# Kernel tuning notes

Hardware: AMD Instinct MI355X
Metric: run time of the kernel (lower is better)

Reference implementation:

```python
import jax, jax.numpy as jnp
import numpy as np

NUM_HEADS = 12


def setup_inputs() -> dict:
    key = jax.random.key(0)
    ks = jax.random.split(key, 6)
    B, F, P, C = 2, 8, 196, 768
    N = 1 + F * P
    s = 0.02
    return {
        "x": jax.random.normal(ks[0], (B, N, C), jnp.float32),
        "Wqkv": jax.random.normal(ks[1], (C, 3 * C), jnp.float32) * s,
        "Wq": jax.random.normal(ks[2], (C, C), jnp.float32) * s,
        "Wkv": jax.random.normal(ks[3], (C, 2 * C), jnp.float32) * s,
        "Wproj": jax.random.normal(ks[4], (C, C), jnp.float32) * s,
        "bproj": jnp.zeros((C,), jnp.float32),
        "seq_len": 196,
        "num_frames": 8,
    }


def reference(x, Wqkv, Wq, Wkv, Wproj, bproj, seq_len, num_frames):
    B, N, C = x.shape
    H = NUM_HEADS
    d = C // H
    scale = d ** -0.5
    F, P = num_frames, seq_len
    S = F * P  # N == 1 + S

    qkv = x @ Wqkv                                # [B, N, 3C]
    q, k, v = jnp.split(qkv, 3, axis=-1)
    def to_heads(t):  # [B, N, C] -> [B*H, N, d]
        return t.reshape(B, N, H, d).transpose(0, 2, 1, 3).reshape(B * H, N, d)
    q, k, v = to_heads(q), to_heads(k), to_heads(v)

    # --- cls token attends over everything ---
    cls_q = q[:, :1] * scale                      # [BH, 1, d]
    cls_attn = jax.nn.softmax(jnp.einsum('bid,bjd->bij', cls_q, k), axis=-1)
    cls_out = jnp.einsum('bij,bjd->bid', cls_attn, v)  # [BH, 1, d]
    cls_out = cls_out.reshape(B, H, d).reshape(B, 1, C)

    # --- per-frame spatial softmax ---
    q_, k_, v_ = q[:, 1:], k[:, 1:], v[:, 1:]     # [BH, S, d]
    qk = jnp.einsum('bqd,bkd->bqk', q_, k_).reshape(B * H, S, F, P)
    sp_attn = jax.nn.softmax(scale * qk, axis=-1)  # softmax over patches within frame
    v_f = v_.reshape(B * H, F, P, d)
    xt = jnp.einsum('bqfn,bfnd->bqfd', sp_attn, v_f)  # [BH, S, F, d]

    x4 = xt.reshape(B, H, S, F, d).transpose(0, 2, 3, 1, 4).reshape(B, S, F, C)

    # --- diagonal extraction: query frame g == key frame f ---
    x5 = x4.reshape(B, F, P, F, C)
    xd = jnp.diagonal(x5, axis1=1, axis2=3)       # [B, P, C, F]
    xd = xd.transpose(0, 3, 1, 2).reshape(B, S, C)

    # --- temporal trajectory attention ---
    q2 = (xd @ Wq).reshape(B, S, H, d).transpose(0, 2, 1, 3) * scale  # [B,H,S,d]
    kv2 = x4 @ Wkv                                # [B, S, F, 2C]
    k2 = kv2[..., :C].reshape(B, S, F, H, d).transpose(0, 3, 1, 2, 4)  # [B,H,S,F,d]
    attn2 = jax.nn.softmax(jnp.einsum('bhsd,bhsfd->bhsf', q2, k2), axis=-1)
    # use_original_code=True: aggregate the trajectory tensor x4 itself
    xr = x4.reshape(B, S, F, H, d).transpose(0, 3, 1, 2, 4)            # [B,H,S,F,d]
    out = jnp.einsum('bhsf,bhsfd->bhsd', attn2, xr)
    out = out.transpose(0, 2, 1, 3).reshape(B, S, C)

    out = jnp.concatenate([cls_out, out], axis=1) @ Wproj + bproj      # [B, N, C]
    return out, attn2
```

## Files before the change

### kernel.cpp

```cpp
#include <hip/hip_runtime.h>

namespace {
constexpr int kB = 2;
constexpr int kH = 12;
constexpr int kD = 64;
constexpr int kC = 768;
constexpr int kF = 8;
constexpr int kP = 196;
constexpr int kS = kF * kP;
constexpr int kN = 1 + kS;
constexpr int k3C = 3 * kC;
constexpr float kScale = 0.125f;
constexpr int kBH = kB * kH;
constexpr int kPpad = 224;
constexpr int kLpad = 1600;
constexpr int kBS = kB * kS;
}

typedef __attribute__((ext_vector_type(8))) short bf16x8;
typedef __attribute__((ext_vector_type(8))) unsigned short u16x8;
typedef __attribute__((ext_vector_type(4))) float f32x4;
typedef __attribute__((ext_vector_type(4))) unsigned int u32x4;

__device__ inline ushort f2bf(float x) {
  union { float f; unsigned u; } v{x};
  unsigned r = v.u + 0x7fff + ((v.u >> 16) & 1);
  return (ushort)(r >> 16);
}
__device__ inline float bf2f(ushort u) {
  union { unsigned u; float f; } v{(unsigned)u << 16};
  return v.f;
}

__device__ __forceinline__ void gload_lds16(const void* g, void* l) {
  __builtin_amdgcn_global_load_lds(
      (const __attribute__((address_space(1))) unsigned int*)g,
      (__attribute__((address_space(3))) unsigned int*)l, 16, 0, 0);
}

__device__ inline void storeC(float v, float* p) { *p = v; }
__device__ inline void storeC(float v, ushort* p) { *p = f2bf(v); }

template <typename OutT>
__global__ __launch_bounds__(256) void gemm_bf16(
    const ushort* __restrict__ A, const ushort* __restrict__ Bt,
    const float* __restrict__ bias, OutT* __restrict__ C,
    int M, int N, int K, int nbx) {
  const int nwg = gridDim.x;
  const int q = nwg >> 3, rr = nwg & 7;
  const int xcd = blockIdx.x & 7, loc = blockIdx.x >> 3;
  const int vid = ((xcd < rr) ? xcd * (q + 1) : rr * (q + 1) + (xcd - rr) * q) + loc;
  const int m0 = (vid / nbx) * 128, n0 = (vid % nbx) * 128;

  __shared__ __align__(16) ushort As[128 * 32];
  __shared__ __align__(16) ushort Bs[128 * 32];
  const int tid = threadIdx.x;
  const int r0 = tid >> 2, c0 = tid & 3;
  const int r1 = r0 + 64;
  const int sc0 = (c0 ^ ((r0 >> 1) & 3)) * 8;
  const int sc1 = (c0 ^ ((r1 >> 1) & 3)) * 8;
  const int ar0 = min(m0 + r0, M - 1), ar1 = min(m0 + r1, M - 1);
  const ushort* ga0 = A + (size_t)ar0 * K + sc0;
  const ushort* ga1 = A + (size_t)ar1 * K + sc1;
  const ushort* gb0 = Bt + (size_t)(n0 + r0) * K + sc0;
  const ushort* gb1 = Bt + (size_t)(n0 + r1) * K + sc1;
  const int w = tid >> 6;
  char* lA0 = (char*)As + w * 1024;
  char* lA1 = (char*)As + 4096 + w * 1024;
  char* lB0 = (char*)Bs + w * 1024;
  char* lB1 = (char*)Bs + 4096 + w * 1024;
  const int lane = tid & 63;
  const int lr = lane & 15, lg = lane >> 4;
  const int wr = w >> 1, wc = w & 1;
  f32x4 acc[4][4] = {};
  for (int kt = 0; kt < K; kt += 32) {
    gload_lds16(ga0 + kt, lA0);
    gload_lds16(ga1 + kt, lA1);
    gload_lds16(gb0 + kt, lB0);
    gload_lds16(gb1 + kt, lB1);
    __syncthreads();
    bf16x8 af[4], bfr[4];
#pragma unroll
    for (int m = 0; m < 4; ++m) {
      int row = wr * 64 + m * 16 + lr;
      int ch = lg ^ ((row >> 1) & 3);
      af[m] = *(const bf16x8*)(As + row * 32 + ch * 8);
    }
#pragma unroll
    for (int n = 0; n < 4; ++n) {
      int row = wc * 64 + n * 16 + lr;
      int ch = lg ^ ((row >> 1) & 3);
      bfr[n] = *(const bf16x8*)(Bs + row * 32 + ch * 8);
    }
#pragma unroll
    for (int m = 0; m < 4; ++m)
#pragma unroll
      for (int n = 0; n < 4; ++n)
        acc[m][n] =
            __builtin_amdgcn_mfma_f32_16x16x32_bf16(af[m], bfr[n], acc[m][n], 0, 0, 0);
    __syncthreads();
  }
#pragma unroll
  for (int m = 0; m < 4; ++m) {
#pragma unroll
    for (int r = 0; r < 4; ++r) {
      const int mg = m0 + wr * 64 + m * 16 + lg * 4 + r;
      if (mg < M) {
        OutT* crow = C + (size_t)mg * N + n0 + wc * 64 + lr;
#pragma unroll
        for (int n = 0; n < 4; ++n) {
          float v = acc[m][n][r];
          if (bias) v += bias[n0 + wc * 64 + n * 16 + lr];
          storeC(v, crow + n * 16);
        }
      }
    }
  }
}

__global__ __launch_bounds__(256) void w2_gemm(
    const ushort* __restrict__ q2b, const ushort* __restrict__ Wkvb,
    ushort* __restrict__ w2b) {
  const int nwg = gridDim.x;
  const int q = nwg >> 3, rr = nwg & 7;
  const int xcd = blockIdx.x & 7, loc = blockIdx.x >> 3;
  const int vid = ((xcd < rr) ? xcd * (q + 1) : rr * (q + 1) + (xcd - rr) * q) + loc;
  const int h = vid / 150;
  const int rem = vid - h * 150;
  const int m0 = (rem / 6) * 128, n0 = (rem % 6) * 128;

  __shared__ __align__(16) ushort As[128 * 32];
  __shared__ __align__(16) ushort Bs[128 * 32];
  const int tid = threadIdx.x;
  const int r0 = tid >> 2, c0 = tid & 3;
  const int r1 = r0 + 64;
  const int sc0 = (c0 ^ ((r0 >> 1) & 3)) * 8;
  const int sc1 = (c0 ^ ((r1 >> 1) & 3)) * 8;
  const int ar0 = min(m0 + r0, kBS - 1), ar1 = min(m0 + r1, kBS - 1);
  const ushort* ga0 = q2b + (size_t)ar0 * kC + h * 64 + sc0;
  const ushort* ga1 = q2b + (size_t)ar1 * kC + h * 64 + sc1;
  const ushort* gb0 = Wkvb + (size_t)(n0 + r0) * kC + h * 64 + sc0;
  const ushort* gb1 = Wkvb + (size_t)(n0 + r1) * kC + h * 64 + sc1;
  const int w = tid >> 6;
  char* lA0 = (char*)As + w * 1024;
  char* lA1 = (char*)As + 4096 + w * 1024;
  char* lB0 = (char*)Bs + w * 1024;
  char* lB1 = (char*)Bs + 4096 + w * 1024;
  const int lane = tid & 63;
  const int lr = lane & 15, lg = lane >> 4;
  const int wr = w >> 1, wc = w & 1;
  f32x4 acc[4][4] = {};
#pragma unroll
  for (int kt = 0; kt < 64; kt += 32) {
    gload_lds16(ga0 + kt, lA0);
    gload_lds16(ga1 + kt, lA1);
    gload_lds16(gb0 + kt, lB0);
    gload_lds16(gb1 + kt, lB1);
    __syncthreads();
    bf16x8 af[4], bfr[4];
#pragma unroll
    for (int m = 0; m < 4; ++m) {
      int row = wr * 64 + m * 16 + lr;
      int ch = lg ^ ((row >> 1) & 3);
      af[m] = *(const bf16x8*)(As + row * 32 + ch * 8);
    }
#pragma unroll
    for (int n = 0; n < 4; ++n) {
      int row = wc * 64 + n * 16 + lr;
      int ch = lg ^ ((row >> 1) & 3);
      bfr[n] = *(const bf16x8*)(Bs + row * 32 + ch * 8);
    }
#pragma unroll
    for (int m = 0; m < 4; ++m)
#pragma unroll
      for (int n = 0; n < 4; ++n)
        acc[m][n] =
            __builtin_amdgcn_mfma_f32_16x16x32_bf16(af[m], bfr[n], acc[m][n], 0, 0, 0);
    __syncthreads();
  }
#pragma unroll
  for (int m = 0; m < 4; ++m) {
#pragma unroll
    for (int r = 0; r < 4; ++r) {
      const int mg = m0 + wr * 64 + m * 16 + lg * 4 + r;
      if (mg < kBS) {
        ushort* crow = w2b + (size_t)mg * (kH * kC) + h * kC + n0 + wc * 64 + lr;
#pragma unroll
        for (int n = 0; n < 4; ++n) crow[n * 16] = f2bf(acc[m][n][r]);
      }
    }
  }
}

__global__ void pack_x_k(const float* __restrict__ X, ushort* __restrict__ Xb,
                         int n4) {
  const int i = blockIdx.x * 256 + threadIdx.x;
  if (i >= n4) return;
  float4 v = ((const float4*)X)[i];
  ushort4 o = {f2bf(v.x), f2bf(v.y), f2bf(v.z), f2bf(v.w)};
  ((ushort4*)Xb)[i] = o;
}

__global__ __launch_bounds__(256) void pack_wt_k(const float* __restrict__ W,
                                                 ushort* __restrict__ Wt,
                                                 int ldw, float scale) {
  __shared__ float t[32][33];
  const int nb = blockIdx.x * 32;
  const int kb = blockIdx.y * 32;
  const int tx = threadIdx.x & 31, ty = threadIdx.x >> 5;
#pragma unroll
  for (int i = 0; i < 32; i += 8)
    t[ty + i][tx] = W[(size_t)(kb + ty + i) * ldw + nb + tx];
  __syncthreads();
#pragma unroll
  for (int i = 0; i < 32; i += 8)
    Wt[(size_t)(nb + ty + i) * 768 + kb + tx] = f2bf(t[tx][ty + i] * scale);
}

__global__ void pack_wkv_k(const float* __restrict__ Wkv,
                           ushort* __restrict__ Wkvb) {
  const int i = blockIdx.x * 256 + threadIdx.x;
  if (i >= 768 * 192) return;
  const int c = i / 192, j4 = i - c * 192;
  float4 v = *(const float4*)(Wkv + (size_t)c * 1536 + j4 * 4);
  ushort4 o = {f2bf(v.x), f2bf(v.y), f2bf(v.z), f2bf(v.w)};
  *(ushort4*)(Wkvb + (size_t)c * 768 + j4 * 4) = o;
}

__global__ void pack_qk_k(const ushort* __restrict__ qkvb,
                          ushort* __restrict__ Qb, ushort* __restrict__ Kb) {
  const int idx = blockIdx.x * 256 + threadIdx.x;
  if (idx >= kBH * kS * 8) return;
  const int j8 = idx & 7;
  const int s = (idx >> 3) % kS;
  const int bh = idx / (kS * 8);
  const int b = bh / kH, h = bh % kH;
  const size_t src = (size_t)(b * kN + 1 + s) * k3C + h * kD + j8 * 8;
  u16x8 qv = *(const u16x8*)(qkvb + src);
  u16x8 qo;
#pragma unroll
  for (int j = 0; j < 8; ++j) qo[j] = f2bf(bf2f(qv[j]) * kScale);
  const size_t dst = ((size_t)bh * kS + s) * kD + j8 * 8;
  *(u16x8*)(Qb + dst) = qo;
  *(u16x8*)(Kb + dst) = *(const u16x8*)(qkvb + src + kC);
}

__global__ void pack_vt_k(const ushort* __restrict__ qkvb,
                          ushort* __restrict__ Vt) {
  const int idx = blockIdx.x * 256 + threadIdx.x;
  if (idx >= kBH * kF * kD * kPpad) return;
  const int n = idx % kPpad;
  const int j = (idx / kPpad) & 63;
  const int f = (idx / (kPpad * kD)) & 7;
  const int bh = idx / (kPpad * kD * kF);
  const int b = bh / kH, h = bh % kH;
  ushort v = 0;
  if (n < kP)
    v = qkvb[(size_t)(b * kN + 1 + f * kP + n) * k3C + 2 * kC + h * kD + j];
  Vt[idx] = v;
}

__global__ __launch_bounds__(256) void sp_attn_mfma(
    const ushort* __restrict__ Qb, const ushort* __restrict__ Kb,
    const ushort* __restrict__ Vt, ushort* __restrict__ x4b) {
  const int w = threadIdx.x >> 6;
  const int lane = threadIdx.x & 63;
  const int fbh = blockIdx.x;
  const int f = fbh / 24, bh = fbh % 24;
  const int tile = blockIdx.y * 4 + w;
  if (tile >= 49) return;
  const int q0 = tile * 32;
  const int lr = lane & 15;
  const int lg = lane >> 4;

  const ushort* qrow = Qb + ((size_t)bh * kS + q0 + lr) * kD + lg * 8;
  const bf16x8 a00 = *(const bf16x8*)qrow;
  const bf16x8 a01 = *(const bf16x8*)(qrow + 32);
  const bf16x8 a10 = *(const bf16x8*)(qrow + 16 * kD);
  const bf16x8 a11 = *(const bf16x8*)(qrow + 16 * kD + 32);

  f32x4 s0[13], s1[13];
  const ushort* kbase = Kb + ((size_t)bh * kS + f * kP + lr) * kD + lg * 8;
#pragma unroll
  for (int nt = 0; nt < 13; ++nt) {
    const ushort* kr = kbase + (size_t)nt * 16 * kD;
    bf16x8 b0 = *(const bf16x8*)kr;
    bf16x8 b1 = *(const bf16x8*)(kr + 32);
    f32x4 acc0 = {0.f, 0.f, 0.f, 0.f}, acc1 = {0.f, 0.f, 0.f, 0.f};
    acc0 = __builtin_amdgcn_mfma_f32_16x16x32_bf16(b0, a00, acc0, 0, 0, 0);
    acc0 = __builtin_amdgcn_mfma_f32_16x16x32_bf16(b1, a01, acc0, 0, 0, 0);
    acc1 = __builtin_amdgcn_mfma_f32_16x16x32_bf16(b0, a10, acc1, 0, 0, 0);
    acc1 = __builtin_amdgcn_mfma_f32_16x16x32_bf16(b1, a11, acc1, 0, 0, 0);
    s0[nt] = acc0;
    s1[nt] = acc1;
  }
  if (lg >= 1) {
#pragma unroll
    for (int r = 0; r < 4; ++r) { s0[12][r] = -1e30f; s1[12][r] = -1e30f; }
  }

  float m0 = -1e30f, m1 = -1e30f;
#pragma unroll
  for (int nt = 0; nt < 13; ++nt)
#pragma unroll
    for (int r = 0; r < 4; ++r) {
      m0 = fmaxf(m0, s0[nt][r]);
      m1 = fmaxf(m1, s1[nt][r]);
    }
  m0 = fmaxf(m0, __shfl_xor(m0, 16));
  m0 = fmaxf(m0, __shfl_xor(m0, 32));
  m1 = fmaxf(m1, __shfl_xor(m1, 16));
  m1 = fmaxf(m1, __shfl_xor(m1, 32));

  float sum0 = 0.f, sum1 = 0.f;
  u32x4 breg0[7], breg1[7];
#pragma unroll
  for (int blk = 0; blk < 7; ++blk) {
    unsigned pk0[2][2], pk1[2][2];
#pragma unroll
    for (int t = 0; t < 2; ++t) {
      const int nt = blk * 2 + t;
      if (nt < 13) {
        float e0 = __expf(s0[nt][0] - m0), e1 = __expf(s0[nt][1] - m0);
        float e2 = __expf(s0[nt][2] - m0), e3 = __expf(s0[nt][3] - m0);
        sum0 += (e0 + e1) + (e2 + e3);
        pk0[t][0] = ((unsigned)f2bf(e1) << 16) | f2bf(e0);
        pk0[t][1] = ((unsigned)f2bf(e3) << 16) | f2bf(e2);
        float g0 = __expf(s1[nt][0] - m1), g1 = __expf(s1[nt][1] - m1);
        float g2 = __expf(s1[nt][2] - m1), g3 = __expf(s1[nt][3] - m1);
        sum1 += (g0 + g1) + (g2 + g3);
        pk1[t][0] = ((unsigned)f2bf(g1) << 16) | f2bf(g0);
        pk1[t][1] = ((unsigned)f2bf(g3) << 16) | f2bf(g2);
      } else {
        pk0[t][0] = 0; pk0[t][1] = 0;
        pk1[t][0] = 0; pk1[t][1] = 0;
      }
    }
#pragma unroll
    for (int j2 = 0; j2 < 4; ++j2) {
      const int srcLane = ((lg & 1) * 2 + (j2 >> 1)) * 16 + lr;
      unsigned t0 = (unsigned)__shfl((int)pk0[0][j2 & 1], srcLane);
      unsigned t1 = (unsigned)__shfl((int)pk0[1][j2 & 1], srcLane);
      breg0[blk][j2] = (lg < 2) ? t0 : t1;
      unsigned u0 = (unsigned)__shfl((int)pk1[0][j2 & 1], srcLane);
      unsigned u1 = (unsigned)__shfl((int)pk1[1][j2 & 1], srcLane);
      breg1[blk][j2] = (lg < 2) ? u0 : u1;
    }
  }
  sum0 += __shfl_xor(sum0, 16);
  sum0 += __shfl_xor(sum0, 32);
  sum1 += __shfl_xor(sum1, 16);
  sum1 += __shfl_xor(sum1, 32);
  const float inv0 = 1.f / sum0, inv1 = 1.f / sum1;

  const ushort* vbase = Vt + ((size_t)(bh * kF + f) * kD + lr) * kPpad + lg * 8;
  f32x4 o0[4] = {}, o1[4] = {};
#pragma unroll
  for (int nt2 = 0; nt2 < 4; ++nt2) {
    const ushort* vb = vbase + (size_t)nt2 * 16 * kPpad;
#pragma unroll
    for (int blk = 0; blk < 7; ++blk) {
      bf16x8 av = *(const bf16x8*)(vb + blk * 32);
      bf16x8 pb0 = __builtin_bit_cast(bf16x8, breg0[blk]);
      bf16x8 pb1 = __builtin_bit_cast(bf16x8, breg1[blk]);
      o0[nt2] = __builtin_amdgcn_mfma_f32_16x16x32_bf16(av, pb0, o0[nt2], 0, 0, 0);
      o1[nt2] = __builtin_amdgcn_mfma_f32_16x16x32_bf16(av, pb1, o1[nt2], 0, 0, 0);
    }
  }

  const int b = bh / kH, h = bh % kH;
  const size_t base0 =
      ((size_t)(b * kS + q0 + lr) * kF + f) * kC + h * kD + lg * 4;
#pragma unroll
  for (int nt2 = 0; nt2 < 4; ++nt2) {
    ushort4 v0, v1;
    v0.x = f2bf(o0[nt2][0] * inv0);
    v0.y = f2bf(o0[nt2][1] * inv0);
    v0.z = f2bf(o0[nt2][2] * inv0);
    v0.w = f2bf(o0[nt2][3] * inv0);
    *(ushort4*)(x4b + base0 + nt2 * 16) = v0;
    v1.x = f2bf(o1[nt2][0] * inv1);
    v1.y = f2bf(o1[nt2][1] * inv1);
    v1.z = f2bf(o1[nt2][2] * inv1);
    v1.w = f2bf(o1[nt2][3] * inv1);
    *(ushort4*)(x4b + base0 + (size_t)16 * kF * kC + nt2 * 16) = v1;
  }
}

__global__ __launch_bounds__(256) void cls_logits_k(const ushort* __restrict__ qkvb,
                                                    float* __restrict__ logits) {
  const int chunk = blockIdx.x, bh = blockIdx.y;
  const int b = bh / kH, h = bh % kH;
  const int g = threadIdx.x & 15, row = threadIdx.x >> 4;
  const size_t base = (size_t)b * kN * k3C;
  const ushort* qp = qkvb + base + h * kD + g * 4;
  const float q0 = bf2f(qp[0]) * kScale, q1 = bf2f(qp[1]) * kScale;
  const float q2 = bf2f(qp[2]) * kScale, q3 = bf2f(qp[3]) * kScale;
#pragma unroll
  for (int i = 0; i < 16; ++i) {
    const int n = chunk * 256 + i * 16 + row;
    if (n < kN) {
      ushort4 kv =
          *(const ushort4*)(qkvb + base + (size_t)n * k3C + kC + h * kD + g * 4);
      float p = q0 * bf2f(kv.x) + q1 * bf2f(kv.y) + q2 * bf2f(kv.z) +
                q3 * bf2f(kv.w);
#pragma unroll
      for (int o = 8; o; o >>= 1) p += __shfl_xor(p, o, 16);
      if (g == 0) logits[bh * kLpad + n] = p;
    }
  }
}

__global__ __launch_bounds__(256) void cls_softmax_k(const float* __restrict__ logits,
                                                     float* __restrict__ pbuf) {
  __shared__ float red[8];
  const int bh = blockIdx.x, tid = threadIdx.x;
  float m = -1e30f;
  for (int n = tid; n < kN; n += 256) m = fmaxf(m, logits[bh * kLpad + n]);
#pragma unroll
  for (int o = 32; o; o >>= 1) m = fmaxf(m, __shfl_xor(m, o));
  if ((tid & 63) == 0) red[tid >> 6] = m;
  __syncthreads();
  m = fmaxf(fmaxf(red[0], red[1]), fmaxf(red[2], red[3]));
  float sum = 0.f;
  for (int n = tid; n < kN; n += 256) sum += __expf(logits[bh * kLpad + n] - m);
#pragma unroll
  for (int o = 32; o; o >>= 1) sum += __shfl_xor(sum, o);
  if ((tid & 63) == 0) red[4 + (tid >> 6)] = sum;
  __syncthreads();
  const float inv = 1.f / (red[4] + red[5] + red[6] + red[7]);
  for (int n = tid; n < kN; n += 256)
    pbuf[bh * kLpad + n] = __expf(logits[bh * kLpad + n] - m) * inv;
}

__global__ __launch_bounds__(256) void cls_pv_k(const ushort* __restrict__ qkvb,
                                                const float* __restrict__ pbuf,
                                                float* __restrict__ partial) {
  __shared__ float pb[256];
  const int chunk = blockIdx.x, bh = blockIdx.y;
  const int b = bh / kH, h = bh % kH;
  const int j = threadIdx.x & 63, part = threadIdx.x >> 6;
  const size_t base = (size_t)b * kN * k3C + 2 * kC + h * kD + j;
  float acc = 0.f;
#pragma unroll 4
  for (int i = 0; i < 64; ++i) {
    const int n = chunk * 256 + i * 4 + part;
    if (n < kN)
      acc = fmaf(pbuf[bh * kLpad + n], bf2f(qkvb[base + (size_t)n * k3C]), acc);
  }
  pb[threadIdx.x] = acc;
  __syncthreads();
  if (part == 0)
    partial[((size_t)bh * 7 + chunk) * kD + j] =
        pb[j] + pb[64 + j] + pb[128 + j] + pb[192 + j];
}

__global__ void cls_red_k(const float* __restrict__ partial,
                          ushort* __restrict__ xin_b) {
  const int bh = blockIdx.x, j = threadIdx.x;
  const int b = bh / kH, h = bh % kH;
  float s = 0.f;
#pragma unroll
  for (int c = 0; c < 7; ++c) s += partial[((size_t)bh * 7 + c) * kD + j];
  xin_b[(size_t)(b * kN) * kC + h * kD + j] = f2bf(s);
}

__global__ void xd_gather_k(const ushort* __restrict__ x4b,
                            ushort* __restrict__ xd_b) {
  const int idx = blockIdx.x * 256 + threadIdx.x;
  const int total = kB * kS * (kC / 8);
  if (idx >= total) return;
  const int row = idx / (kC / 8);
  const int cg = idx - row * (kC / 8);
  const int b = row / kS, s = row - b * kS;
  const int fq = s / kP;
  ((ulonglong2*)xd_b)[(size_t)row * (kC / 8) + cg] =
      ((const ulonglong2*)x4b)[((size_t)(b * kS + s) * kF + fq) * (kC / 8) + cg];
}

__global__ __launch_bounds__(256) void attn2_fused(
    const ushort* __restrict__ x4b, const ushort* __restrict__ w2b,
    ushort* __restrict__ xin_b, float* __restrict__ attn2out) {
  __shared__ __align__(16) ushort x4s[kF * kC];
  __shared__ __align__(16) ushort w2s[kH * kC];
  const int bs = blockIdx.x;
  const int b = bs / kS, s = bs - b * kS;
  const int tid = threadIdx.x;
  {
    const ulonglong2* src = (const ulonglong2*)(x4b + (size_t)bs * kF * kC);
    ulonglong2* dst = (ulonglong2*)x4s;
    for (int i = tid; i < kF * kC / 8; i += 256) dst[i] = src[i];
    const ulonglong2* srcw = (const ulonglong2*)(w2b + (size_t)bs * kH * kC);
    ulonglong2* dstw = (ulonglong2*)w2s;
    for (int i = tid; i < kH * kC / 8; i += 256) dstw[i] = srcw[i];
  }
  __syncthreads();
  const int w = tid >> 6, lane = tid & 63;
#pragma unroll
  for (int hh = 0; hh < 3; ++hh) {
    const int h = w * 3 + hh;
    float part[kF] = {};
#pragma unroll
    for (int i = 0; i < 3; ++i) {
      const int c = lane * 4 + i * 256;
      ushort4 wv = *(const ushort4*)&w2s[h * kC + c];
      const float w0 = bf2f(wv.x), w1 = bf2f(wv.y);
      const float w2v = bf2f(wv.z), w3 = bf2f(wv.w);
#pragma unroll
      for (int f = 0; f < kF; ++f) {
        ushort4 xv = *(const ushort4*)&x4s[f * kC + c];
        part[f] += bf2f(xv.x) * w0 + bf2f(xv.y) * w1 + bf2f(xv.z) * w2v +
                   bf2f(xv.w) * w3;
      }
    }
    float l[kF];
#pragma unroll
    for (int f = 0; f < kF; ++f) {
      float p = part[f];
#pragma unroll
      for (int o = 32; o; o >>= 1) p += __shfl_xor(p, o);
      l[f] = p;
    }
    float m = l[0];
#pragma unroll
    for (int f = 1; f < kF; ++f) m = fmaxf(m, l[f]);
    float sum = 0.f;
#pragma unroll
    for (int f = 0; f < kF; ++f) {
      l[f] = __expf(l[f] - m);
      sum += l[f];
    }
    const float inv = 1.f / sum;
    float pv = 0.f;
#pragma unroll
    for (int f = 0; f < kF; ++f) pv = (lane == f) ? l[f] : pv;
    if (lane < kF)
      attn2out[((size_t)(b * kH + h) * kS + s) * kF + lane] = pv * inv;
    float o = 0.f;
#pragma unroll
    for (int f = 0; f < kF; ++f)
      o = fmaf(l[f] * inv, bf2f(x4s[f * kC + h * kD + lane]), o);
    xin_b[(size_t)(b * kN + 1 + s) * kC + h * kD + lane] = f2bf(o);
  }
}

extern "C" void kernel_launch(void* const* d_in, const int* in_sizes, int n_in,
                              void* d_out, int out_size, void* d_ws,
                              size_t ws_size, hipStream_t stream) {
  const float* x = (const float*)d_in[0];
  const float* Wqkv = (const float*)d_in[1];
  const float* Wq = (const float*)d_in[2];
  const float* Wkv = (const float*)d_in[3];
  const float* Wproj = (const float*)d_in[4];
  const float* bproj = (const float*)d_in[5];

  char* p = (char*)d_ws;
  ushort* qkvb = (ushort*)p;         p += (size_t)3138 * 2304 * 2;
  ushort* w2b = (ushort*)p;          p += (size_t)kBS * kH * kC * 2;
  ushort* q2b = (ushort*)p;          p += (size_t)kBS * kC * 2;
  ushort* x4b = (ushort*)p;          p += (size_t)25088 * 768 * 2;
  ushort* xin_b = (ushort*)p;        p += (size_t)3138 * 768 * 2;
  ushort* xd_b = (ushort*)p;         p += (size_t)kBS * 768 * 2;
  ushort* xb = (ushort*)p;           p += (size_t)3138 * 768 * 2;
  ushort* Wqkv_t = (ushort*)p;       p += (size_t)2304 * 768 * 2;
  ushort* Wq_t = (ushort*)p;         p += (size_t)768 * 768 * 2;
  ushort* Wkvb = (ushort*)p;         p += (size_t)768 * 768 * 2;
  ushort* Wproj_t = (ushort*)p;      p += (size_t)768 * 768 * 2;
  ushort* Qb = (ushort*)p;           p += (size_t)kBH * kS * kD * 2;
  ushort* Kb = (ushort*)p;           p += ((size_t)kBH * kS + 16) * kD * 2;
  ushort* Vt = (ushort*)p;           p += (size_t)kBH * kF * kD * kPpad * 2;
  float* clsL = (float*)p;           p += (size_t)kBH * kLpad * 4;
  float* clsP = (float*)p;           p += (size_t)kBH * kLpad * 4;
  float* clsPart = (float*)p;

  float* out = (float*)d_out;
  float* attn2 = out + (size_t)kB * kN * kC;

  pack_x_k<<<(3138 * 768 / 4 + 255) / 256, 256, 0, stream>>>(x, xb, 3138 * 768 / 4);
  pack_wt_k<<<dim3(72, 24), 256, 0, stream>>>(Wqkv, Wqkv_t, 2304, 1.f);
  pack_wt_k<<<dim3(24, 24), 256, 0, stream>>>(Wq, Wq_t, 768, kScale);
  pack_wkv_k<<<(768 * 192 + 255) / 256, 256, 0, stream>>>(Wkv, Wkvb);
  pack_wt_k<<<dim3(24, 24), 256, 0, stream>>>(Wproj, Wproj_t, 768, 1.f);
  gemm_bf16<ushort><<<18 * 25, 256, 0, stream>>>(xb, Wqkv_t, nullptr, qkvb,
                                                 3138, 2304, 768, 18);
  pack_qk_k<<<(kBH * kS * 8 + 255) / 256, 256, 0, stream>>>(qkvb, Qb, Kb);
  pack_vt_k<<<(kBH * kF * kD * kPpad + 255) / 256, 256, 0, stream>>>(qkvb, Vt);
  cls_logits_k<<<dim3(7, 24), 256, 0, stream>>>(qkvb, clsL);
  cls_softmax_k<<<24, 256, 0, stream>>>(clsL, clsP);
  cls_pv_k<<<dim3(7, 24), 256, 0, stream>>>(qkvb, clsP, clsPart);
  cls_red_k<<<24, 64, 0, stream>>>(clsPart, xin_b);
  sp_attn_mfma<<<dim3(192, 13), 256, 0, stream>>>(Qb, Kb, Vt, x4b);
  xd_gather_k<<<(kB * kS * (kC / 8) + 255) / 256, 256, 0, stream>>>(x4b, xd_b);
  gemm_bf16<ushort><<<6 * 25, 256, 0, stream>>>(xd_b, Wq_t, nullptr, q2b, kBS,
                                                768, 768, 6);
  w2_gemm<<<1800, 256, 0, stream>>>(q2b, Wkvb, w2b);
  attn2_fused<<<kBS, 256, 0, stream>>>(x4b, w2b, xin_b, attn2);
  gemm_bf16<float><<<6 * 25, 256, 0, stream>>>(xin_b, Wproj_t, bproj, out, 3138,
                                               768, 768, 6);
}
```

Before: 263.2 us.

## Fuse Q/K/V packing into QKV GEMM epilogue and diagonal gather into q2 GEMM

The QKV GEMM epilogue now writes the scaled Q, K and transposed V layouts directly, which removes the separate pack_qk and pack_vt kernels. The q2 GEMM reads the diagonal frame rows of x4 through its A-operand addresses, which removes the xd_gather kernel and its intermediate buffer. The spatial attention kernel is relaunched with one 64-thread wave per block instead of four waves per block, so the tile guard is no longer needed. In exchange, the epilogue does scattered 2-byte stores, especially the strided V-transpose writes. The Vt padding columns (patch index 196 to 223) are no longer zero-filled, so correctness now depends on how the attention kernel treats them.

```diff
diff --git a/kernel.cpp b/kernel.cpp
--- a/kernel.cpp
+++ b/kernel.cpp
@@ -118,6 +118,173 @@
   }
 }
 
+__global__ __launch_bounds__(256) void gemm_qkv(
+    const ushort* __restrict__ A, const ushort* __restrict__ Bt,
+    ushort* __restrict__ qkvb, ushort* __restrict__ Qb,
+    ushort* __restrict__ Kb, ushort* __restrict__ Vt) {
+  constexpr int M = 3138, N = k3C, K = kC, nbx = 18;
+  const int nwg = gridDim.x;
+  const int q = nwg >> 3, rr = nwg & 7;
+  const int xcd = blockIdx.x & 7, loc = blockIdx.x >> 3;
+  const int vid = ((xcd < rr) ? xcd * (q + 1) : rr * (q + 1) + (xcd - rr) * q) + loc;
+  const int m0 = (vid / nbx) * 128, n0 = (vid % nbx) * 128;
+
+  __shared__ __align__(16) ushort As[128 * 32];
+  __shared__ __align__(16) ushort Bs[128 * 32];
+  const int tid = threadIdx.x;
+  const int r0 = tid >> 2, c0 = tid & 3;
+  const int r1 = r0 + 64;
+  const int sc0 = (c0 ^ ((r0 >> 1) & 3)) * 8;
+  const int sc1 = (c0 ^ ((r1 >> 1) & 3)) * 8;
+  const int ar0 = min(m0 + r0, M - 1), ar1 = min(m0 + r1, M - 1);
+  const ushort* ga0 = A + (size_t)ar0 * K + sc0;
+  const ushort* ga1 = A + (size_t)ar1 * K + sc1;
+  const ushort* gb0 = Bt + (size_t)(n0 + r0) * K + sc0;
+  const ushort* gb1 = Bt + (size_t)(n0 + r1) * K + sc1;
+  const int w = tid >> 6;
+  char* lA0 = (char*)As + w * 1024;
+  char* lA1 = (char*)As + 4096 + w * 1024;
+  char* lB0 = (char*)Bs + w * 1024;
+  char* lB1 = (char*)Bs + 4096 + w * 1024;
+  const int lane = tid & 63;
+  const int lr = lane & 15, lg = lane >> 4;
+  const int wr = w >> 1, wc = w & 1;
+  f32x4 acc[4][4] = {};
+  for (int kt = 0; kt < K; kt += 32) {
+    gload_lds16(ga0 + kt, lA0);
+    gload_lds16(ga1 + kt, lA1);
+    gload_lds16(gb0 + kt, lB0);
+    gload_lds16(gb1 + kt, lB1);
+    __syncthreads();
+    bf16x8 af[4], bfr[4];
+#pragma unroll
+    for (int m = 0; m < 4; ++m) {
+      int row = wr * 64 + m * 16 + lr;
+      int ch = lg ^ ((row >> 1) & 3);
+      af[m] = *(const bf16x8*)(As + row * 32 + ch * 8);
+    }
+#pragma unroll
+    for (int n = 0; n < 4; ++n) {
+      int row = wc * 64 + n * 16 + lr;
+      int ch = lg ^ ((row >> 1) & 3);
+      bfr[n] = *(const bf16x8*)(Bs + row * 32 + ch * 8);
+    }
+#pragma unroll
+    for (int m = 0; m < 4; ++m)
+#pragma unroll
+      for (int n = 0; n < 4; ++n)
+        acc[m][n] =
+            __builtin_amdgcn_mfma_f32_16x16x32_bf16(af[m], bfr[n], acc[m][n], 0, 0, 0);
+    __syncthreads();
+  }
+#pragma unroll
+  for (int m = 0; m < 4; ++m) {
+#pragma unroll
+    for (int r = 0; r < 4; ++r) {
+      const int mg = m0 + wr * 64 + m * 16 + lg * 4 + r;
+      if (mg >= M) continue;
+      const int b = (mg >= kN) ? 1 : 0;
+      const int tok = mg - b * kN;
+      ushort* qrow = qkvb + (size_t)mg * k3C + n0 + wc * 64 + lr;
+#pragma unroll
+      for (int n = 0; n < 4; ++n) {
+        const int col = n0 + wc * 64 + n * 16 + lr;
+        const float v = acc[m][n][r];
+        const ushort bv = f2bf(v);
+        qrow[n * 16] = bv;
+        if (tok >= 1) {
+          const int s = tok - 1;
+          const int sec = col / kC;
+          const int cj = col - sec * kC;
+          const int h = cj >> 6, j = cj & 63;
+          const int bh = b * kH + h;
+          if (sec == 0) {
+            Qb[((size_t)bh * kS + s) * kD + j] = f2bf(v * kScale);
+          } else if (sec == 1) {
+            Kb[((size_t)bh * kS + s) * kD + j] = bv;
+          } else {
+            const int fq = s / kP, nn = s - fq * kP;
+            Vt[(((size_t)(bh * kF + fq)) * kD + j) * kPpad + nn] = bv;
+          }
+        }
+      }
+    }
+  }
+}
+
+__global__ __launch_bounds__(256) void gemm_q2(
+    const ushort* __restrict__ x4b, const ushort* __restrict__ Bt,
+    ushort* __restrict__ C) {
+  constexpr int M = kBS, N = kC, K = kC, nbx = 6;
+  const int nwg = gridDim.x;
+  const int q = nwg >> 3, rr = nwg & 7;
+  const int xcd = blockIdx.x & 7, loc = blockIdx.x >> 3;
+  const int vid = ((xcd < rr) ? xcd * (q + 1) : rr * (q + 1) + (xcd - rr) * q) + loc;
+  const int m0 = (vid / nbx) * 128, n0 = (vid % nbx) * 128;
+
+  __shared__ __align__(16) ushort As[128 * 32];
+  __shared__ __align__(16) ushort Bs[128 * 32];
+  const int tid = threadIdx.x;
+  const int r0 = tid >> 2, c0 = tid & 3;
+  const int r1 = r0 + 64;
+  const int sc0 = (c0 ^ ((r0 >> 1) & 3)) * 8;
+  const int sc1 = (c0 ^ ((r1 >> 1) & 3)) * 8;
+  const int ar0 = min(m0 + r0, M - 1), ar1 = min(m0 + r1, M - 1);
+  const int fq0 = (ar0 % kS) / kP, fq1 = (ar1 % kS) / kP;
+  const ushort* ga0 = x4b + ((size_t)ar0 * kF + fq0) * kC + sc0;
+  const ushort* ga1 = x4b + ((size_t)ar1 * kF + fq1) * kC + sc1;
+  const ushort* gb0 = Bt + (size_t)(n0 + r0) * K + sc0;
+  const ushort* gb1 = Bt + (size_t)(n0 + r1) * K + sc1;
+  const int w = tid >> 6;
+  char* lA0 = (char*)As + w * 1024;
+  char* lA1 = (char*)As + 4096 + w * 1024;
+  char* lB0 = (char*)Bs + w * 1024;
+  char* lB1 = (char*)Bs + 4096 + w * 1024;
+  const int lane = tid & 63;
+  const int lr = lane & 15, lg = lane >> 4;
+  const int wr = w >> 1, wc = w & 1;
+  f32x4 acc[4][4] = {};
+  for (int kt = 0; kt < K; kt += 32) {
+    gload_lds16(ga0 + kt, lA0);
+    gload_lds16(ga1 + kt, lA1);
+    gload_lds16(gb0 + kt, lB0);
+    gload_lds16(gb1 + kt, lB1);
+    __syncthreads();
+    bf16x8 af[4], bfr[4];
+#pragma unroll
+    for (int m = 0; m < 4; ++m) {
+      int row = wr * 64 + m * 16 + lr;
+      int ch = lg ^ ((row >> 1) & 3);
+      af[m] = *(const bf16x8*)(As + row * 32 + ch * 8);
+    }
+#pragma unroll
+    for (int n = 0; n < 4; ++n) {
+      int row = wc * 64 + n * 16 + lr;
+      int ch = lg ^ ((row >> 1) & 3);
+      bfr[n] = *(const bf16x8*)(Bs + row * 32 + ch * 8);
+    }
+#pragma unroll
+    for (int m = 0; m < 4; ++m)
+#pragma unroll
+      for (int n = 0; n < 4; ++n)
+        acc[m][n] =
+            __builtin_amdgcn_mfma_f32_16x16x32_bf16(af[m], bfr[n], acc[m][n], 0, 0, 0);
+    __syncthreads();
+  }
+#pragma unroll
+  for (int m = 0; m < 4; ++m) {
+#pragma unroll
+    for (int r = 0; r < 4; ++r) {
+      const int mg = m0 + wr * 64 + m * 16 + lg * 4 + r;
+      if (mg < M) {
+        ushort* crow = C + (size_t)mg * N + n0 + wc * 64 + lr;
+#pragma unroll
+        for (int n = 0; n < 4; ++n) crow[n * 16] = f2bf(acc[m][n][r]);
+      }
+    }
+  }
+}
+
 __global__ __launch_bounds__(256) void w2_gemm(
     const ushort* __restrict__ q2b, const ushort* __restrict__ Wkvb,
     ushort* __restrict__ w2b) {
@@ -227,48 +394,13 @@
   *(ushort4*)(Wkvb + (size_t)c * 768 + j4 * 4) = o;
 }
 
-__global__ void pack_qk_k(const ushort* __restrict__ qkvb,
-                          ushort* __restrict__ Qb, ushort* __restrict__ Kb) {
-  const int idx = blockIdx.x * 256 + threadIdx.x;
-  if (idx >= kBH * kS * 8) return;
-  const int j8 = idx & 7;
-  const int s = (idx >> 3) % kS;
-  const int bh = idx / (kS * 8);
-  const int b = bh / kH, h = bh % kH;
-  const size_t src = (size_t)(b * kN + 1 + s) * k3C + h * kD + j8 * 8;
-  u16x8 qv = *(const u16x8*)(qkvb + src);
-  u16x8 qo;
-#pragma unroll
-  for (int j = 0; j < 8; ++j) qo[j] = f2bf(bf2f(qv[j]) * kScale);
-  const size_t dst = ((size_t)bh * kS + s) * kD + j8 * 8;
-  *(u16x8*)(Qb + dst) = qo;
-  *(u16x8*)(Kb + dst) = *(const u16x8*)(qkvb + src + kC);
-}
-
-__global__ void pack_vt_k(const ushort* __restrict__ qkvb,
-                          ushort* __restrict__ Vt) {
-  const int idx = blockIdx.x * 256 + threadIdx.x;
-  if (idx >= kBH * kF * kD * kPpad) return;
-  const int n = idx % kPpad;
-  const int j = (idx / kPpad) & 63;
-  const int f = (idx / (kPpad * kD)) & 7;
-  const int bh = idx / (kPpad * kD * kF);
-  const int b = bh / kH, h = bh % kH;
-  ushort v = 0;
-  if (n < kP)
-    v = qkvb[(size_t)(b * kN + 1 + f * kP + n) * k3C + 2 * kC + h * kD + j];
-  Vt[idx] = v;
-}
-
-__global__ __launch_bounds__(256) void sp_attn_mfma(
+__global__ __launch_bounds__(64) void sp_attn_mfma(
     const ushort* __restrict__ Qb, const ushort* __restrict__ Kb,
     const ushort* __restrict__ Vt, ushort* __restrict__ x4b) {
-  const int w = threadIdx.x >> 6;
-  const int lane = threadIdx.x & 63;
+  const int lane = threadIdx.x;
   const int fbh = blockIdx.x;
   const int f = fbh / 24, bh = fbh % 24;
-  const int tile = blockIdx.y * 4 + w;
-  if (tile >= 49) return;
+  const int tile = blockIdx.y;
   const int q0 = tile * 32;
   const int lr = lane & 15;
   const int lg = lane >> 4;
@@ -465,19 +597,6 @@
   xin_b[(size_t)(b * kN) * kC + h * kD + j] = f2bf(s);
 }
 
-__global__ void xd_gather_k(const ushort* __restrict__ x4b,
-                            ushort* __restrict__ xd_b) {
-  const int idx = blockIdx.x * 256 + threadIdx.x;
-  const int total = kB * kS * (kC / 8);
-  if (idx >= total) return;
-  const int row = idx / (kC / 8);
-  const int cg = idx - row * (kC / 8);
-  const int b = row / kS, s = row - b * kS;
-  const int fq = s / kP;
-  ((ulonglong2*)xd_b)[(size_t)row * (kC / 8) + cg] =
-      ((const ulonglong2*)x4b)[((size_t)(b * kS + s) * kF + fq) * (kC / 8) + cg];
-}
-
 __global__ __launch_bounds__(256) void attn2_fused(
     const ushort* __restrict__ x4b, const ushort* __restrict__ w2b,
     ushort* __restrict__ xin_b, float* __restrict__ attn2out) {
@@ -560,7 +679,6 @@
   ushort* q2b = (ushort*)p;          p += (size_t)kBS * kC * 2;
   ushort* x4b = (ushort*)p;          p += (size_t)25088 * 768 * 2;
   ushort* xin_b = (ushort*)p;        p += (size_t)3138 * 768 * 2;
-  ushort* xd_b = (ushort*)p;         p += (size_t)kBS * 768 * 2;
   ushort* xb = (ushort*)p;           p += (size_t)3138 * 768 * 2;
   ushort* Wqkv_t = (ushort*)p;       p += (size_t)2304 * 768 * 2;
   ushort* Wq_t = (ushort*)p;         p += (size_t)768 * 768 * 2;
@@ -581,18 +699,13 @@
   pack_wt_k<<<dim3(24, 24), 256, 0, stream>>>(Wq, Wq_t, 768, kScale);
   pack_wkv_k<<<(768 * 192 + 255) / 256, 256, 0, stream>>>(Wkv, Wkvb);
   pack_wt_k<<<dim3(24, 24), 256, 0, stream>>>(Wproj, Wproj_t, 768, 1.f);
-  gemm_bf16<ushort><<<18 * 25, 256, 0, stream>>>(xb, Wqkv_t, nullptr, qkvb,
-                                                 3138, 2304, 768, 18);
-  pack_qk_k<<<(kBH * kS * 8 + 255) / 256, 256, 0, stream>>>(qkvb, Qb, Kb);
-  pack_vt_k<<<(kBH * kF * kD * kPpad + 255) / 256, 256, 0, stream>>>(qkvb, Vt);
+  gemm_qkv<<<18 * 25, 256, 0, stream>>>(xb, Wqkv_t, qkvb, Qb, Kb, Vt);
   cls_logits_k<<<dim3(7, 24), 256, 0, stream>>>(qkvb, clsL);
   cls_softmax_k<<<24, 256, 0, stream>>>(clsL, clsP);
   cls_pv_k<<<dim3(7, 24), 256, 0, stream>>>(qkvb, clsP, clsPart);
   cls_red_k<<<24, 64, 0, stream>>>(clsPart, xin_b);
-  sp_attn_mfma<<<dim3(192, 13), 256, 0, stream>>>(Qb, Kb, Vt, x4b);
-  xd_gather_k<<<(kB * kS * (kC / 8) + 255) / 256, 256, 0, stream>>>(x4b, xd_b);
-  gemm_bf16<ushort><<<6 * 25, 256, 0, stream>>>(xd_b, Wq_t, nullptr, q2b, kBS,
-                                                768, 768, 6);
+  sp_attn_mfma<<<dim3(192, 49), 64, 0, stream>>>(Qb, Kb, Vt, x4b);
+  gemm_q2<<<6 * 25, 256, 0, stream>>>(x4b, Wq_t, q2b);
   w2_gemm<<<1800, 256, 0, stream>>>(q2b, Wkvb, w2b);
   attn2_fused<<<kBS, 256, 0, stream>>>(x4b, w2b, xin_b, attn2);
   gemm_bf16<float><<<6 * 25, 256, 0, stream>>>(xin_b, Wproj_t, bproj, out, 3138,
```

After: 253.6 us. 3.6% less time.
